# Kernel tuning notes

Measured on AMD Instinct MI355X. Metric: run time of the kernel, lower is better.

The kernel has to match this reference:

```python
import jax, jax.numpy as jnp
import numpy as np

SCORE_THR = 0.3
NMS_IOU = 0.3
TOPK = 100          # fixed candidate budget replacing dynamic boolean masking
IMAGE_SHAPE = (512, 512)  # (H, W); letterbox_image=False so scale is direct


def pool_nms(heat):
    # 3x3 max-pool peak-NMS: keep only local maxima
    pooled = jax.lax.reduce_window(heat, -jnp.inf, jax.lax.max,
                                   (1, 1, 3, 3), (1, 1, 1, 1), 'SAME')
    return heat * (pooled == heat).astype(heat.dtype)


def setup_inputs() -> dict:
    key = jax.random.key(0)
    k1, k2, k3 = jax.random.split(key, 3)
    hm = jax.random.uniform(k1, (32, 80, 128, 128), dtype=jnp.float32)
    wh = jax.random.uniform(k2, (32, 2, 128, 128), dtype=jnp.float32) * 8.0
    offset = jax.random.uniform(k3, (32, 2, 128, 128), dtype=jnp.float32)
    return {"hm": hm, "wh": wh, "offset": offset}


def reference(hm, wh, offset):
    B, C, H, W = hm.shape
    HW = H * W
    heat = pool_nms(hm)
    heat = heat.transpose(0, 2, 3, 1).reshape(B, HW, C)       # [B,HW,C]
    whf = wh.transpose(0, 2, 3, 1).reshape(B, HW, 2)           # [B,HW,2]
    off = offset.transpose(0, 2, 3, 1).reshape(B, HW, 2)       # [B,HW,2]

    conf = heat.max(-1)                                        # [B,HW]
    cls = jnp.argmax(heat, -1)                                 # [B,HW]

    idx = jnp.arange(HW)
    xv = (idx % W).astype(hm.dtype)
    yv = (idx // W).astype(hm.dtype)
    cx = xv[None, :] + off[..., 0]
    cy = yv[None, :] + off[..., 1]
    bw = whf[..., 0]
    bh = whf[..., 1]
    # normalized xyxy boxes, as in decode_bbox
    boxes = jnp.stack([(cx - bw / 2) / W, (cy - bh / 2) / H,
                       (cx + bw / 2) / W, (cy + bh / 2) / H], -1)  # [B,HW,4]

    scores = jnp.where(conf > SCORE_THR, conf, 0.0)
    top_s, top_i = jax.lax.top_k(scores, TOPK)                 # sorted desc
    tb = jnp.take_along_axis(boxes, top_i[..., None], axis=1)  # [B,K,4]
    tc = jnp.take_along_axis(cls, top_i, axis=1)               # [B,K]
    valid = top_s > SCORE_THR                                  # [B,K]

    # per-class greedy NMS on score-sorted candidates (fixed size K)
    area = (tb[..., 2] - tb[..., 0]) * (tb[..., 3] - tb[..., 1])
    lt = jnp.maximum(tb[:, :, None, :2], tb[:, None, :, :2])
    rb = jnp.minimum(tb[:, :, None, 2:], tb[:, None, :, 2:])
    whi = jnp.clip(rb - lt, 0.0)
    inter = whi[..., 0] * whi[..., 1]
    iou = inter / (area[:, :, None] + area[:, None, :] - inter + 1e-9)
    supmat = (iou > NMS_IOU) & (tc[:, :, None] == tc[:, None, :])  # [B,K,K]

    j = jnp.arange(TOPK)

    def body(i, keep):
        alive_i = jnp.take(keep, i, axis=1)[:, None]           # [B,1]
        sup = jnp.take(supmat, i, axis=1) & (j[None, :] > i) & alive_i
        return keep & ~sup

    keep = jax.lax.fori_loop(0, TOPK, body, valid)             # [B,K]

    # centernet_correct_boxes with letterbox_image=False: scale to image size
    ih, iw = IMAGE_SHAPE
    cxy = (tb[..., :2] + tb[..., 2:]) / 2
    cwh = tb[..., 2:] - tb[..., :2]
    mins = cxy - cwh / 2
    maxs = cxy + cwh / 2
    scale = jnp.array([iw, ih, iw, ih], hm.dtype)
    bimg = jnp.concatenate([mins, maxs], -1) * scale           # [B,K,4]

    dets = jnp.concatenate([bimg, top_s[..., None],
                            tc[..., None].astype(hm.dtype)], -1)  # [B,K,6]
    return jnp.where(keep[..., None], dets, 0.0)
```

## Files before the change

kernel.cpp:

```cpp
#include <hip/hip_runtime.h>
#include <hip/hip_bf16.h>
#include <stdint.h>

#define HH 128
#define WW 128
#define CC 80
#define HW (HH * WW)
#define BB 32
#define TOPK 100
#define NTHREADS 256
#define SCORE_THR 0.3f
#define NMS_IOU 0.3f
#define BUF 512
#define GG 4
#define PLANE ((size_t)BB * HW)
#define MINT 0x3E99999Bu

__global__ __launch_bounds__(NTHREADS, 8)
void heat_reduce(const float* __restrict__ hm,
                 float* __restrict__ conf_part,
                 unsigned char* __restrict__ cls_part) {
    constexpr int CPG = CC / GG;
    const int stripe = blockIdx.x & 15;
    const int g      = (blockIdx.x >> 4) & 3;
    const int b      = blockIdx.x >> 6;
    const int tid    = threadIdx.x;
    const int c31    = tid & 31;
    const int r      = tid >> 5;
    const int x4     = c31 << 2;
    const int y      = stripe * 8 + r;
    const int yM     = (y > 0) ? y - 1 : 0;
    const int yP     = (y < HH - 1) ? y + 1 : y;
    const bool leftClamp  = (c31 == 0);
    const bool rightClamp = (c31 == 31);
    const int c0     = g * CPG;

    const float* cbase = hm + (size_t)(b * CC + c0) * HW;
    const uint o0 = (uint)(yM * WW + x4);
    const uint o1 = (uint)(y  * WW + x4);
    const uint o2 = (uint)(yP * WW + x4);

    float conf[4] = {0.f, 0.f, 0.f, 0.f};
    int   cls[4]  = {c0, c0, c0, c0};

    auto rowmax = [&](float4 a, float rm[4]) {
        float le = __shfl_up(a.w, 1, 64);
        float re = __shfl_down(a.x, 1, 64);
        if (leftClamp)  le = a.x;
        if (rightClamp) re = a.w;
        rm[0] = fmaxf(fmaxf(le,  a.x), a.y);
        rm[1] = fmaxf(fmaxf(a.x, a.y), a.z);
        rm[2] = fmaxf(fmaxf(a.y, a.z), a.w);
        rm[3] = fmaxf(fmaxf(a.z, a.w), re);
    };

    float4 n0 = *(const float4*)(cbase + o0);
    float4 n1 = *(const float4*)(cbase + o1);
    float4 n2 = *(const float4*)(cbase + o2);

    for (int cc = 0; cc < CPG; ++cc) {
        float4 a0 = n0, a1 = n1, a2 = n2;
        if (cc + 1 < CPG) {
            cbase += HW;
            n0 = *(const float4*)(cbase + o0);
            n1 = *(const float4*)(cbase + o1);
            n2 = *(const float4*)(cbase + o2);
        }
        float rm0[4], rm1[4], rm2[4];
        rowmax(a0, rm0);
        rowmax(a1, rm1);
        rowmax(a2, rm2);
        float ctr[4] = {a1.x, a1.y, a1.z, a1.w};
        const int c = c0 + cc;
#pragma unroll
        for (int i = 0; i < 4; ++i) {
            float pool = fmaxf(fmaxf(rm0[i], rm1[i]), rm2[i]);
            float heat = (ctr[i] == pool) ? ctr[i] : 0.0f;
            if (heat > conf[i]) { conf[i] = heat; cls[i] = c; }
        }
    }

    size_t idx = (size_t)g * PLANE + (size_t)b * HW + (size_t)y * WW + x4;
    *(float4*)&conf_part[idx] = make_float4(conf[0], conf[1], conf[2], conf[3]);
    *(uchar4*)&cls_part[idx]  = make_uchar4((unsigned char)cls[0],
                                            (unsigned char)cls[1],
                                            (unsigned char)cls[2],
                                            (unsigned char)cls[3]);
}

__global__ __launch_bounds__(NTHREADS, 1)
void select_nms(const float* __restrict__ conf_part,
                const unsigned char* __restrict__ cls_part,
                const float* __restrict__ wh,
                const float* __restrict__ offset,
                float* __restrict__ out) {
    const int b    = blockIdx.x;
    const int tid  = threadIdx.x;
    const int lane = tid & 63;
    const int wid  = tid >> 6;
    constexpr int VALS = HW / NTHREADS;

    __shared__ int wsum[4];
    __shared__ unsigned int sCnt;
    __shared__ unsigned long long keys[BUF];

    unsigned u[VALS];
#pragma unroll
    for (int k = 0; k < VALS; ++k) {
        size_t base = (size_t)b * HW + (k * NTHREADS + tid);
        float s0 = conf_part[base];
        float s1 = conf_part[PLANE + base];
        float s2 = conf_part[2 * PLANE + base];
        float s3 = conf_part[3 * PLANE + base];
        float best = fmaxf(fmaxf(s0, s1), fmaxf(s2, s3));
        u[k] = (best > SCORE_THR) ? __float_as_uint(best) : 0u;
    }

    auto blockCount = [&](unsigned T) -> int {
        int c = 0;
#pragma unroll
        for (int k = 0; k < VALS; ++k) c += (u[k] >= T);
        for (int o = 32; o > 0; o >>= 1) c += __shfl_down(c, o, 64);
        if (lane == 0) wsum[wid] = c;
        __syncthreads();
        int tot = wsum[0] + wsum[1] + wsum[2] + wsum[3];
        __syncthreads();
        return tot;
    };

    unsigned V;
    {
        unsigned lo = MINT, hi = 0x3F800001u;
        int cl = blockCount(lo);
        if (cl < TOPK) {
            V = lo;
        } else {
            while (hi - lo > 1u) {
                unsigned mid = lo + ((hi - lo) >> 1);
                if (blockCount(mid) >= TOPK) lo = mid; else hi = mid;
            }
            V = lo;
        }
    }

    if (tid == 0) sCnt = 0;
    for (int i = tid; i < BUF; i += NTHREADS) keys[i] = 0ull;
    __syncthreads();
#pragma unroll
    for (int k = 0; k < VALS; ++k) {
        if (u[k] >= V) {
            int i = k * NTHREADS + tid;
            unsigned pos = atomicAdd(&sCnt, 1u);
            if (pos < BUF)
                keys[pos] = ((unsigned long long)u[k] << 32) |
                            (unsigned)(HW - 1 - i);
        }
    }
    __syncthreads();
    int cnt = (int)sCnt;
    if (cnt > BUF) cnt = BUF;

    int n = 1;
    while (n < cnt) n <<= 1;
    for (int k = 2; k <= n; k <<= 1) {
        for (int j = k >> 1; j > 0; j >>= 1) {
            for (int i = tid; i < n; i += NTHREADS) {
                int p = i ^ j;
                if (p > i) {
                    unsigned long long a = keys[i], bb2 = keys[p];
                    bool asc_seg = ((i & k) != 0);
                    bool sw = asc_seg ? (a > bb2) : (a < bb2);
                    if (sw) { keys[i] = bb2; keys[p] = a; }
                }
            }
            __syncthreads();
        }
    }

    __shared__ float bx[TOPK][4];
    __shared__ float barea[TOPK];
    __shared__ float bsc[TOPK];
    __shared__ int   bcls[TOPK];
    __shared__ int   keep[TOPK];

    if (tid < TOPK) {
        unsigned long long kk = keys[tid];
        float sc = __uint_as_float((unsigned)(kk >> 32));
        int   i  = HW - 1 - (int)(kk & 0xFFFFFFFFull);
        int   y  = (i >> 7) & 127;
        int   x  = i & 127;
        size_t base0 = (size_t)b * HW + i;
        float bcf = conf_part[base0];
        int   bc  = (int)cls_part[base0];
#pragma unroll
        for (int gg = 1; gg < GG; ++gg) {
            float cf = conf_part[gg * PLANE + base0];
            if (cf > bcf) { bcf = cf; bc = (int)cls_part[gg * PLANE + base0]; }
        }

        size_t base = (size_t)b * 2 * HW + (size_t)y * WW + x;
        float ox = offset[base];
        float oy = offset[base + HW];
        float w  = wh[base];
        float hh = wh[base + HW];
        float cx = (float)x + ox;
        float cy = (float)y + oy;
        float x1 = (cx - w  * 0.5f) * (1.0f / 128.0f);
        float y1 = (cy - hh * 0.5f) * (1.0f / 128.0f);
        float x2 = (cx + w  * 0.5f) * (1.0f / 128.0f);
        float y2 = (cy + hh * 0.5f) * (1.0f / 128.0f);
        bx[tid][0] = x1; bx[tid][1] = y1; bx[tid][2] = x2; bx[tid][3] = y2;
        barea[tid] = (x2 - x1) * (y2 - y1);
        bsc[tid]   = sc;
        bcls[tid]  = bc;
        keep[tid]  = (sc > SCORE_THR) ? 1 : 0;
    }
    __syncthreads();

    if (tid < 64) {
        const int A  = tid;
        const int Bq = tid + 64;
        float aX0 = bx[A][0], aY0 = bx[A][1], aX1 = bx[A][2], aY1 = bx[A][3];
        float aAr = barea[A]; int aC = bcls[A]; int kA = keep[A];
        float bX0 = 0, bY0 = 0, bX1 = 0, bY1 = 0, bAr = 0;
        int   bC = -1, kB = 0;
        if (Bq < TOPK) {
            bX0 = bx[Bq][0]; bY0 = bx[Bq][1]; bX1 = bx[Bq][2]; bY1 = bx[Bq][3];
            bAr = barea[Bq]; bC = bcls[Bq]; kB = keep[Bq];
        }
        for (int i = 0; i < TOPK; ++i) {
            int kv    = (i < 64) ? kA : kB;
            int alive = __shfl(kv, i & 63, 64);
            if (alive) {
                float iX0 = bx[i][0], iY0 = bx[i][1];
                float iX1 = bx[i][2], iY1 = bx[i][3];
                float iAr = barea[i]; int iC = bcls[i];
                if (A > i && aC == iC) {
                    float lx = fmaxf(aX0, iX0), ly = fmaxf(aY0, iY0);
                    float rx = fminf(aX1, iX1), ry = fminf(aY1, iY1);
                    float iw = fmaxf(rx - lx, 0.f), ih = fmaxf(ry - ly, 0.f);
                    float inter = iw * ih;
                    float iou = inter / (aAr + iAr - inter + 1e-9f);
                    if (iou > NMS_IOU) kA = 0;
                }
                if (Bq > i && Bq < TOPK && bC == iC) {
                    float lx = fmaxf(bX0, iX0), ly = fmaxf(bY0, iY0);
                    float rx = fminf(bX1, iX1), ry = fminf(bY1, iY1);
                    float iw = fmaxf(rx - lx, 0.f), ih = fmaxf(ry - ly, 0.f);
                    float inter = iw * ih;
                    float iou = inter / (bAr + iAr - inter + 1e-9f);
                    if (iou > NMS_IOU) kB = 0;
                }
            }
        }
        keep[A] = kA;
        if (Bq < TOPK) keep[Bq] = kB;
    }
    __syncthreads();

    for (int t = tid; t < TOPK * 6; t += NTHREADS) {
        int j = t / 6, comp = t - j * 6;
        float v = 0.0f;
        if (keep[j]) {
            if (comp < 4)       v = bx[j][comp] * 512.0f;
            else if (comp == 4) v = bsc[j];
            else                v = (float)bcls[j];
        }
        out[(size_t)b * (TOPK * 6) + t] = v;
    }
}

extern "C" void kernel_launch(void* const* d_in, const int* in_sizes, int n_in,
                              void* d_out, int out_size, void* d_ws, size_t ws_size,
                              hipStream_t stream) {
    const float* hm     = (const float*)d_in[0];
    const float* wh     = (const float*)d_in[1];
    const float* offset = (const float*)d_in[2];
    float* out = (float*)d_out;

    float* confp = (float*)d_ws;
    unsigned char* clsp = (unsigned char*)d_ws + GG * PLANE * 4;

    heat_reduce<<<BB * GG * 16, NTHREADS, 0, stream>>>(hm, confp, clsp);
    select_nms<<<BB, NTHREADS, 0, stream>>>(confp, clsp, wh, offset, out);
}
```

Baseline: 292.3 us.

## Prefetch two channels ahead and pool vertically before horizontal shuffles

The heat-reduction kernel now keeps a three-slot register ring and prefetches channel planes two iterations ahead, up from one, in a fully unrolled channel loop. It takes the vertical max across the three rows first and then does a single horizontal shuffle pass, so each channel needs two lane shuffles instead of six. The peak test is folded into one combined compare per pixel. The aim is to hide more HBM latency and cut ALU and shuffle work, at the cost of more registers, which could lower occupancy.

```diff
diff --git a/kernel.cpp b/kernel.cpp
--- a/kernel.cpp
+++ b/kernel.cpp
@@ -43,41 +43,47 @@
     float conf[4] = {0.f, 0.f, 0.f, 0.f};
     int   cls[4]  = {c0, c0, c0, c0};
 
-    auto rowmax = [&](float4 a, float rm[4]) {
-        float le = __shfl_up(a.w, 1, 64);
-        float re = __shfl_down(a.x, 1, 64);
-        if (leftClamp)  le = a.x;
-        if (rightClamp) re = a.w;
-        rm[0] = fmaxf(fmaxf(le,  a.x), a.y);
-        rm[1] = fmaxf(fmaxf(a.x, a.y), a.z);
-        rm[2] = fmaxf(fmaxf(a.y, a.z), a.w);
-        rm[3] = fmaxf(fmaxf(a.z, a.w), re);
+    float4 A[3][3];
+
+    auto ld = [&](int cc, int s) {
+        const uint co = (uint)(cc * HW);
+        A[s][0] = *(const float4*)(cbase + (co + o0));
+        A[s][1] = *(const float4*)(cbase + (co + o1));
+        A[s][2] = *(const float4*)(cbase + (co + o2));
     };
 
-    float4 n0 = *(const float4*)(cbase + o0);
-    float4 n1 = *(const float4*)(cbase + o1);
-    float4 n2 = *(const float4*)(cbase + o2);
-
+    auto cmp = [&](int cc, int s) {
+        float vx = fmaxf(fmaxf(A[s][0].x, A[s][1].x), A[s][2].x);
+        float vy = fmaxf(fmaxf(A[s][0].y, A[s][1].y), A[s][2].y);
+        float vz = fmaxf(fmaxf(A[s][0].z, A[s][1].z), A[s][2].z);
+        float vw = fmaxf(fmaxf(A[s][0].w, A[s][1].w), A[s][2].w);
+        float le = __shfl_up(vw, 1, 64);
+        float re = __shfl_down(vx, 1, 64);
+        if (leftClamp)  le = vx;
+        if (rightClamp) re = vw;
+        float p0 = fmaxf(fmaxf(le, vx), vy);
+        float p1 = fmaxf(fmaxf(vx, vy), vz);
+        float p2 = fmaxf(fmaxf(vy, vz), vw);
+        float p3 = fmaxf(fmaxf(vz, vw), re);
+        const int c = c0 + cc;
+        float c0v = A[s][1].x, c1v = A[s][1].y;
+        float c2v = A[s][1].z, c3v = A[s][1].w;
+        bool k0 = (c0v == p0) && (c0v > conf[0]);
+        bool k1 = (c1v == p1) && (c1v > conf[1]);
+        bool k2 = (c2v == p2) && (c2v > conf[2]);
+        bool k3 = (c3v == p3) && (c3v > conf[3]);
+        if (k0) { conf[0] = c0v; cls[0] = c; }
+        if (k1) { conf[1] = c1v; cls[1] = c; }
+        if (k2) { conf[2] = c2v; cls[2] = c; }
+        if (k3) { conf[3] = c3v; cls[3] = c; }
+    };
+
+    ld(0, 0);
+    ld(1, 1);
+#pragma unroll
     for (int cc = 0; cc < CPG; ++cc) {
-        float4 a0 = n0, a1 = n1, a2 = n2;
-        if (cc + 1 < CPG) {
-            cbase += HW;
-            n0 = *(const float4*)(cbase + o0);
-            n1 = *(const float4*)(cbase + o1);
-            n2 = *(const float4*)(cbase + o2);
-        }
-        float rm0[4], rm1[4], rm2[4];
-        rowmax(a0, rm0);
-        rowmax(a1, rm1);
-        rowmax(a2, rm2);
-        float ctr[4] = {a1.x, a1.y, a1.z, a1.w};
-        const int c = c0 + cc;
-#pragma unroll
-        for (int i = 0; i < 4; ++i) {
-            float pool = fmaxf(fmaxf(rm0[i], rm1[i]), rm2[i]);
-            float heat = (ctr[i] == pool) ? ctr[i] : 0.0f;
-            if (heat > conf[i]) { conf[i] = heat; cls[i] = c; }
-        }
+        if (cc + 2 < CPG) ld(cc + 2, (cc + 2) % 3);
+        cmp(cc, cc % 3);
     }
 
     size_t idx = (size_t)g * PLANE + (size_t)b * HW + (size_t)y * WW + x4;
```

Measured after the change: 368.6 us. 26.1% more time.
